# Kernel tuning notes

Hardware: AMD Instinct MI355X
Metric: run time of the kernel (lower is better)

Reference implementation:

```python
import jax, jax.numpy as jnp
import numpy as np

H, HK, HD = 6, 2, 128  # n_heads, n_kv_heads, head_dim (from AcousticTransformerArgs defaults)


def setup_inputs() -> dict:
    key = jax.random.key(0)
    k1, k2, k3, k4, k5 = jax.random.split(key, 5)
    B, S, D = 2, 4096, 768
    s = 0.02
    return {
        "x": jax.random.normal(k1, (B, S, D), dtype=jnp.float32),
        "wq": jax.random.normal(k2, (H * HD, D), dtype=jnp.float32) * s,
        "wk": jax.random.normal(k3, (HK * HD, D), dtype=jnp.float32) * s,
        "wv": jax.random.normal(k4, (HK * HD, D), dtype=jnp.float32) * s,
        "wo": jax.random.normal(k5, (D, H * HD), dtype=jnp.float32) * s,
    }


def reference(x, wq, wk, wv, wo):
    B, S, D = x.shape
    rep = H // HK  # GQA repeat factor (3)
    scale = 1.0 / jnp.sqrt(jnp.asarray(HD, x.dtype))
    # projections (torch Linear: y = x @ W^T)
    q = (x @ wq.T).reshape(B, S, HK, rep, HD) * scale  # head h = g*rep + r
    k = (x @ wk.T).reshape(B, S, HK, HD)
    v = (x @ wv.T).reshape(B, S, HK, HD)
    # bidirectional (no mask) attention with GQA broadcast instead of physical repeat
    scores = jnp.einsum("bsgrd,btgd->bgrst", q, k)  # [B,HK,rep,S,S]
    attn = jax.nn.softmax(scores, axis=-1)
    out = jnp.einsum("bgrst,btgd->bsgrd", attn, v).reshape(B, S, H * HD)
    return out @ wo.T
```

## Files before the change

kernel.cpp:

```cpp
#include <hip/hip_runtime.h>
#include <hip/hip_bf16.h>
#include <type_traits>

using bf16 = __hip_bfloat16;
typedef __attribute__((ext_vector_type(8))) short bf16x8;
typedef __attribute__((ext_vector_type(4))) float floatx4;

static constexpr int Bb = 2, S = 4096, D = 768, H = 6, HK = 2, HD = 128, REP = 3;
static constexpr int M_ROWS = Bb * S;
static constexpr int NQKV = 1280;

__device__ __forceinline__ floatx4 mfma16(bf16x8 a, bf16x8 b, floatx4 c) {
  return __builtin_amdgcn_mfma_f32_16x16x32_bf16(a, b, c, 0, 0, 0);
}

__device__ __forceinline__ void gld_lds16(const bf16* g, bf16* l) {
  __builtin_amdgcn_global_load_lds(
      (const __attribute__((address_space(1))) unsigned int*)g,
      (__attribute__((address_space(3))) unsigned int*)l, 16, 0, 0);
}

#if defined(__has_builtin)
#if __has_builtin(__builtin_amdgcn_exp2f)
#define EXP2F(x) __builtin_amdgcn_exp2f(x)
#endif
#endif
#ifndef EXP2F
#define EXP2F(x) exp2f(x)
#endif

__device__ __forceinline__ unsigned pk2(float a, float b) {
  unsigned ua = __builtin_bit_cast(unsigned, a) + 0x8000u;
  unsigned ub = __builtin_bit_cast(unsigned, b) + 0x8000u;
#if defined(__has_builtin) && __has_builtin(__builtin_amdgcn_perm)
  return __builtin_amdgcn_perm(ub, ua, 0x07060302);
#else
  return (ua >> 16) | (ub & 0xffff0000u);
#endif
}

__device__ __forceinline__ void perm32swap(unsigned& a, unsigned& b) {
  asm volatile("v_permlane32_swap_b32 %0, %1" : "+v"(a), "+v"(b));
}
__device__ __forceinline__ void perm16swap(unsigned& a, unsigned& b) {
  asm volatile("v_permlane16_swap_b32 %0, %1" : "+v"(a), "+v"(b));
}

static constexpr size_t E_X  = (size_t)M_ROWS * D;
static constexpr size_t E_WQ = E_X + (size_t)H * HD * D;
static constexpr size_t E_WK = E_WQ + (size_t)HK * HD * D;
static constexpr size_t E_WV = E_WK + (size_t)HK * HD * D;
static constexpr size_t E_WO = E_WV + (size_t)D * H * HD;

__global__ __launch_bounds__(256) void cvt_all(const float* __restrict__ x,
                                               const float* __restrict__ wq,
                                               const float* __restrict__ wk,
                                               const float* __restrict__ wv,
                                               const float* __restrict__ wo,
                                               bf16* __restrict__ xb,
                                               bf16* __restrict__ wqkvb,
                                               bf16* __restrict__ wob, float qscale) {
  size_t i = ((size_t)blockIdx.x * 256 + threadIdx.x) * 4;
  const float* src;
  bf16* dst;
  float s = 1.f;
  size_t off;
  if (i < E_X)        { src = x;  dst = xb;                 off = i; }
  else if (i < E_WQ)  { src = wq; dst = wqkvb;              off = i - E_X; s = qscale; }
  else if (i < E_WK)  { src = wk; dst = wqkvb + 589824;     off = i - E_WQ; }
  else if (i < E_WV)  { src = wv; dst = wqkvb + 786432;     off = i - E_WK; }
  else                { src = wo; dst = wob;                off = i - E_WV; }
  float4 v = *(const float4*)(src + off);
  uint2 st;
  st.x = pk2(v.x * s, v.y * s);
  st.y = pk2(v.z * s, v.w * s);
  *(uint2*)(dst + off) = st;
}

template <typename OutT, bool VT_FUSE>
__global__ __launch_bounds__(256, 3) void gemm_bt(const bf16* __restrict__ A,
                                                  const bf16* __restrict__ W,
                                                  OutT* __restrict__ C,
                                                  bf16* __restrict__ Vt,
                                                  int M, int N, int K) {
  const int tid = threadIdx.x;
  const int wave = tid >> 6, lane = tid & 63;
  const int quad = lane >> 4, lq = lane & 15;
  const int m0 = blockIdx.x * 128, n0 = blockIdx.y * 128;
  const int wm = (wave & 1) * 64, wn = (wave >> 1) * 64;

  __shared__ __align__(16) bf16 As[128 * 64];
  __shared__ __align__(16) bf16 Ws[128 * 64];

  floatx4 acc[4][4] = {};

  const int srow = lane >> 3, sc = lane & 7;

  for (int k0 = 0; k0 < K; k0 += 64) {
#pragma unroll
    for (int i = 0; i < 4; ++i) {
      int ig = wave * 4 + i;
      int r = ig * 8 + srow;
      int c = sc ^ (r & 7);
      gld_lds16(&A[(size_t)(m0 + r) * K + k0 + c * 8], &As[ig * 512]);
      gld_lds16(&W[(size_t)(n0 + r) * K + k0 + c * 8], &Ws[ig * 512]);
    }
    __syncthreads();
#pragma unroll
    for (int kh = 0; kh < 2; ++kh) {
      bf16x8 af[4], wf[4];
#pragma unroll
      for (int i = 0; i < 4; ++i) {
        int ra = wm + i * 16 + lq, rw = wn + i * 16 + lq;
        af[i] = *(const bf16x8*)&As[ra * 64 + (((kh * 4 + quad) ^ (ra & 7)) * 8)];
        wf[i] = *(const bf16x8*)&Ws[rw * 64 + (((kh * 4 + quad) ^ (rw & 7)) * 8)];
      }
#pragma unroll
      for (int i = 0; i < 4; ++i)
#pragma unroll
        for (int j = 0; j < 4; ++j) acc[i][j] = mfma16(af[i], wf[j], acc[i][j]);
    }
    __syncthreads();
  }

  if (VT_FUSE && n0 >= 1024) {
    bf16* tb = (wave < 2 ? As : Ws) + (wave & 1) * 4096;
    char* tc = (char*)tb;
#pragma unroll
    for (int i = 0; i < 4; ++i)
#pragma unroll
      for (int j = 0; j < 4; ++j) {
        uint2 st;
        st.x = pk2(acc[i][j][0], acc[i][j][1]);
        st.y = pk2(acc[i][j][2], acc[i][j][3]);
        int col = j * 16 + lq;
        int cc = (i * 2 + (quad >> 1)) ^ (col & 7);
        *(uint2*)(tc + col * 128 + cc * 16 + (quad & 1) * 8) = st;
      }
    const int b = m0 >> 12;
    const int dd_off = lane >> 3, schunk = lane & 7;
    const int sbase = (m0 & 4095) + wm + schunk * 8;
#pragma unroll
    for (int e = 0; e < 8; ++e) {
      int cl = e * 8 + dd_off;
      int col = (n0 - 1024) + wn + cl;
      int gg = col >> 7, dd = col & 127;
      bf16x8 vv = *(const bf16x8*)(tc + cl * 128 + ((schunk ^ (cl & 7)) * 16));
      *(bf16x8*)&Vt[((size_t)(b * HK + gg) * HD + dd) * S + sbase] = vv;
    }
    return;
  }
#pragma unroll
  for (int i = 0; i < 4; ++i)
#pragma unroll
    for (int j = 0; j < 4; ++j)
#pragma unroll
      for (int r = 0; r < 4; ++r) {
        int row = m0 + wm + i * 16 + quad * 4 + r;
        int col = n0 + wn + j * 16 + lq;
        float v = acc[i][j][r];
        if constexpr (std::is_same_v<OutT, float>)
          C[(size_t)row * N + col] = v;
        else
          C[(size_t)row * N + col] = __float2bfloat16(v);
      }
}

__global__ __launch_bounds__(256, 3) void gemm_out(const bf16* __restrict__ A,
                                                   const bf16* __restrict__ W,
                                                   float* __restrict__ C,
                                                   int M, int N, int K) {
  const int tid = threadIdx.x;
  const int wave = tid >> 6, lane = tid & 63;
  const int quad = lane >> 4, lq = lane & 15;
  const int m0 = blockIdx.x * 128, n0 = blockIdx.y * 64;
  const int wm = (wave & 1) * 64, wn = (wave >> 1) * 32;

  __shared__ __align__(16) bf16 As[128 * 64];
  __shared__ __align__(16) bf16 Ws[64 * 64];

  floatx4 acc[4][2] = {};

  const int srow = lane >> 3, sc = lane & 7;

  for (int k0 = 0; k0 < K; k0 += 64) {
#pragma unroll
    for (int i = 0; i < 4; ++i) {
      int ig = wave * 4 + i;
      int r = ig * 8 + srow;
      int c = sc ^ (r & 7);
      gld_lds16(&A[(size_t)(m0 + r) * K + k0 + c * 8], &As[ig * 512]);
    }
#pragma unroll
    for (int i = 0; i < 2; ++i) {
      int ig = wave * 2 + i;
      int r = ig * 8 + srow;
      int c = sc ^ (r & 7);
      gld_lds16(&W[(size_t)(n0 + r) * K + k0 + c * 8], &Ws[ig * 512]);
    }
    __syncthreads();
#pragma unroll
    for (int kh = 0; kh < 2; ++kh) {
      bf16x8 af[4], wf[2];
#pragma unroll
      for (int i = 0; i < 4; ++i) {
        int ra = wm + i * 16 + lq;
        af[i] = *(const bf16x8*)&As[ra * 64 + (((kh * 4 + quad) ^ (ra & 7)) * 8)];
      }
#pragma unroll
      for (int j = 0; j < 2; ++j) {
        int rw = wn + j * 16 + lq;
        wf[j] = *(const bf16x8*)&Ws[rw * 64 + (((kh * 4 + quad) ^ (rw & 7)) * 8)];
      }
#pragma unroll
      for (int i = 0; i < 4; ++i)
#pragma unroll
        for (int j = 0; j < 2; ++j) acc[i][j] = mfma16(af[i], wf[j], acc[i][j]);
    }
    __syncthreads();
  }
#pragma unroll
  for (int i = 0; i < 4; ++i)
#pragma unroll
    for (int j = 0; j < 2; ++j)
#pragma unroll
      for (int r = 0; r < 4; ++r) {
        int row = m0 + wm + i * 16 + quad * 4 + r;
        int col = n0 + wn + j * 16 + lq;
        C[(size_t)row * N + col] = acc[i][j][r];
      }
}

__global__ __launch_bounds__(256, 2) void flash_attn(const bf16* __restrict__ QKV,
                                                     const bf16* __restrict__ Vt,
                                                     bf16* __restrict__ O) {
  const int bid = blockIdx.x;
  const int bg = (bid & 7) >> 1;
  const int b = bg >> 1, g = bg & 1;
  const int qt = ((bid >> 3) << 1) | (bid & 1);
  const int q0 = qt * 32;

  const int tid = threadIdx.x;
  const int w = tid >> 6, lane = tid & 63;
  const int half = w >> 1, wp = w & 1;
  const int quad = lane >> 4, lq = lane & 15;

  __shared__ __align__(16) char smem[65536];
  bf16* Ks = (bf16*)smem;
  bf16* Vs = (bf16*)(smem + 32768);

  const bf16* Kgh = QKV + (size_t)b * S * NQKV + H * HD + g * HD + (size_t)half * 2048 * NQKV;
  const bf16* Vgh = Vt + (size_t)(b * HK + g) * HD * S + half * 2048;

  auto stage = [&](int t0, int buf) {
    bf16* kd = Ks + (buf * 2 + half) * 4096;
    bf16* vd = Vs + (buf * 2 + half) * 4096;
#pragma unroll
    for (int i = 0; i < 4; ++i) {
      int ig = wp * 4 + i;
      int tl = ig * 4 + (lane >> 4);
      int c = (lane & 15) ^ (tl & 15);
      gld_lds16(Kgh + (size_t)(t0 + tl) * NQKV + c * 8, kd + ig * 512);
    }
#pragma unroll
    for (int i = 0; i < 4; ++i) {
      int ig = wp * 4 + i;
      int dl = ig * 16 + (lane >> 2);
      int c = (lane & 3) ^ ((dl >> 1) & 3);
      gld_lds16(Vgh + (size_t)dl * S + t0 + c * 8, vd + ig * 512);
    }
  };

  stage(0, 0);

  const bf16* Qg = QKV + ((size_t)b * S + q0 + wp * 16 + lq) * NQKV + g * REP * HD;
  bf16x8 qf[3][4];
#pragma unroll
  for (int u = 0; u < 3; ++u)
#pragma unroll
    for (int kk = 0; kk < 4; ++kk)
      qf[u][kk] = *(const bf16x8*)(Qg + u * HD + kk * 32 + quad * 8);

  bf16x8 ones;
#pragma unroll
  for (int j = 0; j < 8; ++j) ones[j] = (short)0x3F80;

  floatx4 o[3][8] = {};
  floatx4 lacc[3] = {};
  const int sw = (lq >> 1) & 3;

#pragma unroll 2
  for (int it = 0; it < 64; ++it) {
    const int cur = it & 1;
    __syncthreads();
    if (it + 1 < 64) stage((it + 1) * 32, cur ^ 1);

    const bf16* ks = Ks + (cur * 2 + half) * 4096;
    const bf16* vs = Vs + (cur * 2 + half) * 4096;

    floatx4 sf[3][2] = {};
    __builtin_amdgcn_s_setprio(1);
#pragma unroll
    for (int tt = 0; tt < 2; ++tt)
#pragma unroll
      for (int kk = 0; kk < 4; ++kk) {
        int c = (kk * 4 + quad) ^ lq;
        bf16x8 kf = *(const bf16x8*)&ks[(tt * 16 + lq) * 128 + c * 8];
#pragma unroll
        for (int u = 0; u < 3; ++u) sf[u][tt] = mfma16(kf, qf[u][kk], sf[u][tt]);
      }
    __builtin_amdgcn_s_setprio(0);

    bf16x8 pf[3];
#pragma unroll
    for (int u = 0; u < 3; ++u) {
      unsigned A0 = pk2(EXP2F(sf[u][0][0]), EXP2F(sf[u][0][1]));
      unsigned A1 = pk2(EXP2F(sf[u][0][2]), EXP2F(sf[u][0][3]));
      unsigned B0 = pk2(EXP2F(sf[u][1][0]), EXP2F(sf[u][1][1]));
      unsigned B1 = pk2(EXP2F(sf[u][1][2]), EXP2F(sf[u][1][3]));
      perm32swap(A0, B0);
      perm16swap(A0, B0);
      perm32swap(A1, B1);
      perm16swap(A1, B1);
      union { unsigned d[4]; bf16x8 v; } pu;
      pu.d[0] = A0; pu.d[1] = A1; pu.d[2] = B0; pu.d[3] = B1;
      pf[u] = pu.v;
    }

    __builtin_amdgcn_s_setprio(1);
#pragma unroll
    for (int u = 0; u < 3; ++u) lacc[u] = mfma16(ones, pf[u], lacc[u]);

#pragma unroll
    for (int dd = 0; dd < 8; ++dd) {
      bf16x8 vf = *(const bf16x8*)&vs[(dd * 16 + lq) * 32 + ((quad ^ sw) * 8)];
#pragma unroll
      for (int u = 0; u < 3; ++u) o[u][dd] = mfma16(vf, pf[u], o[u][dd]);
    }
    __builtin_amdgcn_s_setprio(0);
  }

  __syncthreads();
  floatx4* oscr = (floatx4*)smem;
  float* lscr = (float*)(smem + 49152);
  if (half == 1) {
#pragma unroll
    for (int u = 0; u < 3; ++u) {
#pragma unroll
      for (int dd = 0; dd < 8; ++dd)
        oscr[((wp * 3 + u) * 8 + dd) * 64 + lane] = o[u][dd];
      lscr[(wp * 3 + u) * 64 + lane] = lacc[u][0];
    }
  }
  __syncthreads();
  if (half == 0) {
    const size_t row = (size_t)b * S + q0 + wp * 16 + lq;
#pragma unroll
    for (int u = 0; u < 3; ++u) {
      float l = lacc[u][0] + lscr[(wp * 3 + u) * 64 + lane];
      float rinv = 1.0f / l;
#pragma unroll
      for (int dd = 0; dd < 8; ++dd) {
        floatx4 oc = o[u][dd] + oscr[((wp * 3 + u) * 8 + dd) * 64 + lane];
        uint2 st;
        st.x = pk2(oc[0] * rinv, oc[1] * rinv);
        st.y = pk2(oc[2] * rinv, oc[3] * rinv);
        int col = (g * REP + u) * HD + dd * 16 + quad * 4;
        *(uint2*)&O[row * (H * HD) + col] = st;
      }
    }
  }
}

static inline size_t al256(size_t x) { return (x + 255) & ~size_t(255); }

extern "C" void kernel_launch(void* const* d_in, const int* in_sizes, int n_in,
                              void* d_out, int out_size, void* d_ws, size_t ws_size,
                              hipStream_t stream) {
  const float* x  = (const float*)d_in[0];
  const float* wq = (const float*)d_in[1];
  const float* wk = (const float*)d_in[2];
  const float* wv = (const float*)d_in[3];
  const float* wo = (const float*)d_in[4];
  float* out = (float*)d_out;

  char* w = (char*)d_ws;
  size_t off = 0;
  auto carve = [&](size_t elems) {
    bf16* p = (bf16*)(w + off);
    off = al256(off + elems * sizeof(bf16));
    return p;
  };
  bf16* xb    = carve((size_t)M_ROWS * D);
  bf16* wqkvb = carve((size_t)NQKV * D);
  bf16* wob   = carve((size_t)D * (H * HD));
  bf16* QKVb  = carve((size_t)M_ROWS * NQKV);
  bf16* Vtb   = carve((size_t)M_ROWS * (HK * HD));
  bf16* Ab    = carve((size_t)M_ROWS * (H * HD));

  const float qscale = 0.1275174465f;

  cvt_all<<<(int)(E_WO / 1024), 256, 0, stream>>>(x, wq, wk, wv, wo, xb, wqkvb, wob, qscale);

  gemm_bt<bf16, true><<<dim3(M_ROWS / 128, NQKV / 128), 256, 0, stream>>>(
      xb, wqkvb, QKVb, Vtb, M_ROWS, NQKV, D);

  flash_attn<<<512, 256, 0, stream>>>(QKVb, Vtb, Ab);

  gemm_out<<<dim3(M_ROWS / 128, D / 64), 256, 0, stream>>>(
      Ab, wob, out, M_ROWS, D, H * HD);
}
```

Measured before the change: 221.8 us.

## Software-pipeline flash attention so PV of previous tile overlaps current QK

Restructures the attention loop so the P·V and row-sum MFMAs for the previous key tile are issued right after the current tile's QK^T MFMAs. The exp/pack work for the current tile can then interleave with independent matrix work instead of stalling the MFMA pipe. V staging moves to a triple buffer so the previous tile's V stays valid while the next one loads, and an epilogue drains the last tile. This grows LDS to 80KB per block and keeps extra P fragments live in registers, which may pressure occupancy at two blocks per CU.

```diff
diff --git a/kernel.cpp b/kernel.cpp
--- a/kernel.cpp
+++ b/kernel.cpp
@@ -245,16 +245,16 @@
   const int half = w >> 1, wp = w & 1;
   const int quad = lane >> 4, lq = lane & 15;
 
-  __shared__ __align__(16) char smem[65536];
+  __shared__ __align__(16) char smem[81920];
   bf16* Ks = (bf16*)smem;
   bf16* Vs = (bf16*)(smem + 32768);
 
   const bf16* Kgh = QKV + (size_t)b * S * NQKV + H * HD + g * HD + (size_t)half * 2048 * NQKV;
   const bf16* Vgh = Vt + (size_t)(b * HK + g) * HD * S + half * 2048;
 
-  auto stage = [&](int t0, int buf) {
-    bf16* kd = Ks + (buf * 2 + half) * 4096;
-    bf16* vd = Vs + (buf * 2 + half) * 4096;
+  auto stage = [&](int t0, int kbuf, int vbuf) {
+    bf16* kd = Ks + (kbuf * 2 + half) * 4096;
+    bf16* vd = Vs + (vbuf * 2 + half) * 4096;
 #pragma unroll
     for (int i = 0; i < 4; ++i) {
       int ig = wp * 4 + i;
@@ -271,7 +271,7 @@
     }
   };
 
-  stage(0, 0);
+  stage(0, 0, 0);
 
   const bf16* Qg = QKV + ((size_t)b * S + q0 + wp * 16 + lq) * NQKV + g * REP * HD;
   bf16x8 qf[3][4];
@@ -287,16 +287,16 @@
 
   floatx4 o[3][8] = {};
   floatx4 lacc[3] = {};
+  bf16x8 pf_prev[3];
   const int sw = (lq >> 1) & 3;
 
 #pragma unroll 2
   for (int it = 0; it < 64; ++it) {
-    const int cur = it & 1;
+    const int kcur = it & 1;
     __syncthreads();
-    if (it + 1 < 64) stage((it + 1) * 32, cur ^ 1);
-
-    const bf16* ks = Ks + (cur * 2 + half) * 4096;
-    const bf16* vs = Vs + (cur * 2 + half) * 4096;
+    if (it + 1 < 64) stage((it + 1) * 32, kcur ^ 1, (it + 1) % 3);
+
+    const bf16* ks = Ks + (kcur * 2 + half) * 4096;
 
     floatx4 sf[3][2] = {};
     __builtin_amdgcn_s_setprio(1);
@@ -309,9 +309,20 @@
 #pragma unroll
         for (int u = 0; u < 3; ++u) sf[u][tt] = mfma16(kf, qf[u][kk], sf[u][tt]);
       }
+
+    if (it) {
+      const bf16* vs = Vs + ((((it - 1) % 3) * 2) + half) * 4096;
+#pragma unroll
+      for (int u = 0; u < 3; ++u) lacc[u] = mfma16(ones, pf_prev[u], lacc[u]);
+#pragma unroll
+      for (int dd = 0; dd < 8; ++dd) {
+        bf16x8 vf = *(const bf16x8*)&vs[(dd * 16 + lq) * 32 + ((quad ^ sw) * 8)];
+#pragma unroll
+        for (int u = 0; u < 3; ++u) o[u][dd] = mfma16(vf, pf_prev[u], o[u][dd]);
+      }
+    }
     __builtin_amdgcn_s_setprio(0);
 
-    bf16x8 pf[3];
 #pragma unroll
     for (int u = 0; u < 3; ++u) {
       unsigned A0 = pk2(EXP2F(sf[u][0][0]), EXP2F(sf[u][0][1]));
@@ -324,20 +335,20 @@
       perm16swap(A1, B1);
       union { unsigned d[4]; bf16x8 v; } pu;
       pu.d[0] = A0; pu.d[1] = A1; pu.d[2] = B0; pu.d[3] = B1;
-      pf[u] = pu.v;
-    }
-
-    __builtin_amdgcn_s_setprio(1);
-#pragma unroll
-    for (int u = 0; u < 3; ++u) lacc[u] = mfma16(ones, pf[u], lacc[u]);
-
+      pf_prev[u] = pu.v;
+    }
+  }
+
+  {
+    const bf16* vs = Vs + (0 * 2 + half) * 4096;
+#pragma unroll
+    for (int u = 0; u < 3; ++u) lacc[u] = mfma16(ones, pf_prev[u], lacc[u]);
 #pragma unroll
     for (int dd = 0; dd < 8; ++dd) {
       bf16x8 vf = *(const bf16x8*)&vs[(dd * 16 + lq) * 32 + ((quad ^ sw) * 8)];
 #pragma unroll
-      for (int u = 0; u < 3; ++u) o[u][dd] = mfma16(vf, pf[u], o[u][dd]);
-    }
-    __builtin_amdgcn_s_setprio(0);
+      for (int u = 0; u < 3; ++u) o[u][dd] = mfma16(vf, pf_prev[u], o[u][dd]);
+    }
   }
 
   __syncthreads();
```

Result: no change. 220.9 us (-0.4%).
